# Optimization experiments

Hardware: AMD Instinct MI355X
Metric: run time of the kernel (lower is better)

## Reference

```python
import jax, jax.numpy as jnp
import numpy as np

EMBED_DIM = 1024
NUM_HEADS = 16
HEAD_DIM = EMBED_DIM // NUM_HEADS
SCALE = HEAD_DIM ** -0.5
B, S = 4, 2048


def setup_inputs() -> dict:
    key = jax.random.key(0)
    ks = jax.random.split(key, 11)
    std = EMBED_DIM ** -0.5
    return {
        "query": jax.random.normal(ks[0], (B, S, EMBED_DIM), jnp.float32),
        "key": jax.random.normal(ks[1], (B, S, EMBED_DIM), jnp.float32),
        "value": jax.random.normal(ks[2], (B, S, EMBED_DIM), jnp.float32),
        "Wq": jax.random.normal(ks[3], (EMBED_DIM, EMBED_DIM), jnp.float32) * std,
        "bq": jax.random.normal(ks[4], (EMBED_DIM,), jnp.float32) * 0.01,
        "Wk": jax.random.normal(ks[5], (EMBED_DIM, EMBED_DIM), jnp.float32) * std,
        "bk": jax.random.normal(ks[6], (EMBED_DIM,), jnp.float32) * 0.01,
        "Wv": jax.random.normal(ks[7], (EMBED_DIM, EMBED_DIM), jnp.float32) * std,
        "bv": jax.random.normal(ks[8], (EMBED_DIM,), jnp.float32) * 0.01,
        "Wo": jax.random.normal(ks[9], (EMBED_DIM, EMBED_DIM), jnp.float32) * std,
        "bo": jax.random.normal(ks[10], (EMBED_DIM,), jnp.float32) * 0.01,
    }


def reference(query, key, value, Wq, bq, Wk, bk, Wv, bv, Wo, bo):
    b, s, _ = query.shape
    # torch.nn.Linear: x @ W.T + b
    q = query @ Wq.T + bq
    k = key @ Wk.T + bk
    v = value @ Wv.T + bv
    # [b, h, s, d]
    q = q.reshape(b, s, NUM_HEADS, HEAD_DIM).transpose(0, 2, 1, 3)
    k = k.reshape(b, s, NUM_HEADS, HEAD_DIM).transpose(0, 2, 1, 3)
    v = v.reshape(b, s, NUM_HEADS, HEAD_DIM).transpose(0, 2, 1, 3)
    # explicit scores [b, h, s, s]
    scores = jnp.einsum("bhqd,bhkd->bhqk", q, k) * SCALE
    causal = jnp.tril(jnp.ones((s, s), dtype=bool))  # is_causal=True
    scores = jnp.where(causal, scores, -jnp.inf)
    attn = jax.nn.softmax(scores, axis=-1)
    out = jnp.einsum("bhqk,bhkd->bhqd", attn, v)
    out = out.transpose(0, 2, 1, 3).reshape(b, s, EMBED_DIM)
    return out @ Wo.T + bo
```

## Files before the change

kernel.cpp:

```cpp
#include <hip/hip_runtime.h>


#define E 1024
#define HEADS 16
#define HD 64
#define SEQ 2048
#define BATCH 4
#define MROWS (BATCH * SEQ)

typedef __bf16 bf16x8 __attribute__((ext_vector_type(8)));
typedef __bf16 bf16x2 __attribute__((ext_vector_type(2)));
typedef float f32x4 __attribute__((ext_vector_type(4)));
typedef unsigned short ushort8v __attribute__((ext_vector_type(8)));

typedef __attribute__((address_space(1))) void gvoid;
typedef __attribute__((address_space(3))) void lvoid;

__device__ __forceinline__ void async16(const void* g, void* l) {
  __builtin_amdgcn_global_load_lds((gvoid*)g, (lvoid*)l, 16, 0, 0);
}

__device__ __forceinline__ unsigned short f2bf(float f) {
  union { float f; unsigned int u; } v;
  v.f = f;
  unsigned int r = v.u + 0x7FFFu + ((v.u >> 16) & 1u);
  return (unsigned short)(r >> 16);
}

__device__ __forceinline__ unsigned packbf(float a, float b) {
  bf16x2 t;
  t[0] = (__bf16)a;
  t[1] = (__bf16)b;
  return __builtin_bit_cast(unsigned, t);
}

__device__ __forceinline__ void store_out(unsigned short* p, float v) { *p = f2bf(v); }
__device__ __forceinline__ void store_out(float* p, float v) { *p = v; }

struct CastArgs {
  const float* src[4];
  unsigned short* dst[4];
  int n;
};

__global__ __launch_bounds__(256) void cast_kernel(CastArgs a) {
  const float* s = a.src[blockIdx.z];
  unsigned short* d = a.dst[blockIdx.z];
  const int n = a.n;
  const int stride = gridDim.x * blockDim.x * 4;
  for (int i = (blockIdx.x * blockDim.x + threadIdx.x) * 4; i < n; i += stride) {
    float4 v = *(const float4*)(s + i);
    ushort4 o;
    o.x = f2bf(v.x); o.y = f2bf(v.y); o.z = f2bf(v.z); o.w = f2bf(v.w);
    *(ushort4*)(d + i) = o;
  }
}

template <typename OutT>
__device__ __forceinline__ void gemm_body(const unsigned short* __restrict__ A,
                                          const unsigned short* __restrict__ W,
                                          const float* __restrict__ bias,
                                          OutT* __restrict__ out, float scale) {
  __shared__ unsigned short At[128 * 64];
  __shared__ unsigned short Wt[128 * 64];
  const int tid = threadIdx.x;
  const int lane = tid & 63;
  const int wv = tid >> 6;
  const int wm = wv & 1, wn = wv >> 1;
  const int li = lane & 15, g = lane >> 4;
  const int m0 = blockIdx.x * 128, n0 = blockIdx.y * 128;
  f32x4 acc[4][4] = {};

  for (int k0 = 0; k0 < E; k0 += 64) {
    __syncthreads();
#pragma unroll
    for (int i = 0; i < 4; ++i) {
      int c = tid + 256 * i;
      int row = c >> 3, slot = c & 7;
      int gc = slot ^ (row & 7);
      async16(A + (size_t)(m0 + row) * E + k0 + gc * 8, &At[c * 8]);
      async16(W + (size_t)(n0 + row) * E + k0 + gc * 8, &Wt[c * 8]);
    }
    asm volatile("s_waitcnt vmcnt(0)" ::: "memory");
    __syncthreads();
#pragma unroll
    for (int kk = 0; kk < 2; ++kk) {
      bf16x8 af[4], bfr[4];
#pragma unroll
      for (int mt = 0; mt < 4; ++mt) {
        int r = wm * 64 + mt * 16 + li;
        int slot = (kk * 4 + g) ^ (r & 7);
        af[mt] = *(const bf16x8*)&At[r * 64 + slot * 8];
      }
#pragma unroll
      for (int nt = 0; nt < 4; ++nt) {
        int r = wn * 64 + nt * 16 + li;
        int slot = (kk * 4 + g) ^ (r & 7);
        bfr[nt] = *(const bf16x8*)&Wt[r * 64 + slot * 8];
      }
#pragma unroll
      for (int mt = 0; mt < 4; ++mt)
#pragma unroll
        for (int nt = 0; nt < 4; ++nt)
          acc[mt][nt] =
              __builtin_amdgcn_mfma_f32_16x16x32_bf16(af[mt], bfr[nt], acc[mt][nt], 0, 0, 0);
    }
  }

#pragma unroll
  for (int nt = 0; nt < 4; ++nt) {
    int col = n0 + wn * 64 + nt * 16 + li;
    float bv = bias[col];
#pragma unroll
    for (int mt = 0; mt < 4; ++mt) {
#pragma unroll
      for (int r = 0; r < 4; ++r) {
        int row = m0 + wm * 64 + mt * 16 + g * 4 + r;
        store_out(&out[(size_t)row * E + col], (acc[mt][nt][r] + bv) * scale);
      }
    }
  }
}

struct QkvArgs {
  const unsigned short* A[3];
  const unsigned short* W[3];
  const float* bias[3];
  unsigned short* out[3];
  float scale[3];
};

__global__ __launch_bounds__(256) void gemm_qkv(QkvArgs p) {
  const int z = blockIdx.z;
  gemm_body<unsigned short>(p.A[z], p.W[z], p.bias[z], p.out[z], p.scale[z]);
}

__global__ __launch_bounds__(256) void gemm_out_k(const unsigned short* __restrict__ A,
                                                  const unsigned short* __restrict__ W,
                                                  const float* __restrict__ bias,
                                                  float* __restrict__ out) {
  gemm_body<float>(A, W, bias, out, 1.0f);
}

__global__ __launch_bounds__(256, 2) void flash_kernel(const unsigned short* __restrict__ Qb,
                                                       const unsigned short* __restrict__ Kb,
                                                       const unsigned short* __restrict__ Vb,
                                                       unsigned short* __restrict__ Ob) {
  __shared__ unsigned short Kt[2][128 * 64];
  __shared__ unsigned short Vt[2][64 * 128];
  const int p = blockIdx.x;
  const int bh = blockIdx.y;
  const int b = bh >> 4, h16 = bh & 15;
  const size_t base = (size_t)b * SEQ * E + (size_t)h16 * HD;
  const unsigned short* Qp = Qb + base;
  const unsigned short* Kp = Kb + base;
  const unsigned short* Vp = Vb + base;
  unsigned short* Op = Ob + base;
  const int tid = threadIdx.x, lane = tid & 63, wv = tid >> 6;
  const int li = lane & 15, g = lane >> 4;
  const int qlo = p, qhi = 15 - p;
  const int slo = ((g & 1) << 5) | li;

  bf16x8 qfL[2][2], qfH[2][2];
#pragma unroll
  for (int mt = 0; mt < 2; ++mt)
#pragma unroll
    for (int kk = 0; kk < 2; ++kk) {
      int rl = qlo * 128 + wv * 32 + mt * 16 + li;
      int rh = qhi * 128 + wv * 32 + mt * 16 + li;
      qfL[mt][kk] = *(const bf16x8*)(Qp + (size_t)rl * E + kk * 32 + g * 8);
      qfH[mt][kk] = *(const bf16x8*)(Qp + (size_t)rh * E + kk * 32 + g * 8);
    }

  f32x4 oaL[4][2] = {}, oaH[4][2] = {};
  float miL[2] = {-1e30f, -1e30f}, lsL[2] = {0.0f, 0.0f};
  float miH[2] = {-1e30f, -1e30f}, lsH[2] = {0.0f, 0.0f};

  ushort8v vv[4];

  auto loadV = [&](int j) {
#pragma unroll
    for (int i = 0; i < 4; ++i) {
      int c = tid + 256 * i;
      int key = c & 127, db = (c >> 7) * 8;
      vv[i] = *(const ushort8v*)(Vp + (size_t)(j * 128 + key) * E + db);
    }
  };
  auto stageK = [&](int j, int buf) {
#pragma unroll
    for (int i = 0; i < 4; ++i) {
      int c = tid + 256 * i;
      int row = c >> 3, slot = c & 7;
      int gc = slot ^ (row & 7);
      async16(Kp + (size_t)(j * 128 + row) * E + gc * 8, &Kt[buf][c * 8]);
    }
  };
  auto scatV = [&](int buf) {
#pragma unroll
    for (int i = 0; i < 4; ++i) {
      int c = tid + 256 * i;
      int key = c & 127, db = (c >> 7) * 8;
#pragma unroll
      for (int jj = 0; jj < 8; ++jj) {
        int n = db + jj;
        int slot = (key >> 3) ^ (n & 15);
        Vt[buf][n * 128 + slot * 8 + (key & 7)] = vv[i][jj];
      }
    }
  };

  auto compute = [&](const bf16x8 (&qf)[2][2], float (&mi)[2], float (&ls)[2],
                     f32x4 (&oa)[4][2], bool diag, int buf) {
#pragma unroll
    for (int h = 0; h < 2; ++h) {
      if (diag && h * 64 > wv * 32 + 31) continue;

      f32x4 sacc[4][2] = {};
#pragma unroll
      for (int kk = 0; kk < 2; ++kk) {
        bf16x8 kf[4];
#pragma unroll
        for (int nt = 0; nt < 4; ++nt) {
          int key = h * 64 + nt * 16 + li;
          int slot = (kk * 4 + g) ^ (key & 7);
          kf[nt] = *(const bf16x8*)&Kt[buf][key * 64 + slot * 8];
        }
#pragma unroll
        for (int nt = 0; nt < 4; ++nt)
#pragma unroll
          for (int mt = 0; mt < 2; ++mt)
            sacc[nt][mt] =
                __builtin_amdgcn_mfma_f32_16x16x32_bf16(kf[nt], qf[mt][kk], sacc[nt][mt], 0, 0, 0);
      }

      if (diag && h * 64 + 63 > wv * 32) {
#pragma unroll
        for (int nt = 0; nt < 4; ++nt)
#pragma unroll
          for (int mt = 0; mt < 2; ++mt)
#pragma unroll
            for (int r = 0; r < 4; ++r) {
              int keyg = h * 64 + nt * 16 + g * 4 + r;
              int qg = wv * 32 + mt * 16 + li;
              sacc[nt][mt][r] = (keyg > qg) ? -1e30f : sacc[nt][mt][r];
            }
      }

      float alpha[2];
#pragma unroll
      for (int mt = 0; mt < 2; ++mt) {
        float mx = sacc[0][mt][0];
#pragma unroll
        for (int nt = 0; nt < 4; ++nt)
#pragma unroll
          for (int r = 0; r < 4; ++r) mx = fmaxf(mx, sacc[nt][mt][r]);
        mx = fmaxf(mx, __shfl_xor(mx, 16));
        mx = fmaxf(mx, __shfl_xor(mx, 32));
        float mnew = fmaxf(mi[mt], mx);
        alpha[mt] = __expf(mi[mt] - mnew);
        mi[mt] = mnew;
      }

      unsigned pk[4][2][2];
      float rs[2] = {0.0f, 0.0f};
#pragma unroll
      for (int nt = 0; nt < 4; ++nt)
#pragma unroll
        for (int mt = 0; mt < 2; ++mt) {
          float p0 = __expf(sacc[nt][mt][0] - mi[mt]);
          float p1 = __expf(sacc[nt][mt][1] - mi[mt]);
          float p2 = __expf(sacc[nt][mt][2] - mi[mt]);
          float p3 = __expf(sacc[nt][mt][3] - mi[mt]);
          rs[mt] += (p0 + p1) + (p2 + p3);
          pk[nt][mt][0] = packbf(p0, p1);
          pk[nt][mt][1] = packbf(p2, p3);
        }
#pragma unroll
      for (int mt = 0; mt < 2; ++mt) {
        float s = rs[mt];
        s += __shfl_xor(s, 16);
        s += __shfl_xor(s, 32);
        ls[mt] = ls[mt] * alpha[mt] + s;
#pragma unroll
        for (int dt = 0; dt < 4; ++dt) oa[dt][mt] *= alpha[mt];
      }

#pragma unroll
      for (int kk2 = 0; kk2 < 2; ++kk2) {
        const int kc = h * 2 + kk2;
        bf16x8 vf[4];
#pragma unroll
        for (int dt = 0; dt < 4; ++dt) {
          int d = dt * 16 + li;
          int slot = (kc * 4 + g) ^ (d & 15);
          vf[dt] = *(const bf16x8*)&Vt[buf][d * 128 + slot * 8];
        }
#pragma unroll
        for (int mt = 0; mt < 2; ++mt) {
          int a0 = __shfl((int)pk[kk2 * 2][mt][0], slo);
          int a1 = __shfl((int)pk[kk2 * 2][mt][1], slo);
          int a2 = __shfl((int)pk[kk2 * 2][mt][0], slo + 16);
          int a3 = __shfl((int)pk[kk2 * 2][mt][1], slo + 16);
          int c0 = __shfl((int)pk[kk2 * 2 + 1][mt][0], slo);
          int c1 = __shfl((int)pk[kk2 * 2 + 1][mt][1], slo);
          int c2 = __shfl((int)pk[kk2 * 2 + 1][mt][0], slo + 16);
          int c3 = __shfl((int)pk[kk2 * 2 + 1][mt][1], slo + 16);
          bool hi = (g & 2) != 0;
          uint4 bb;
          bb.x = hi ? c0 : a0;
          bb.y = hi ? c1 : a1;
          bb.z = hi ? c2 : a2;
          bb.w = hi ? c3 : a3;
          bf16x8 pf = __builtin_bit_cast(bf16x8, bb);
#pragma unroll
          for (int dt = 0; dt < 4; ++dt)
            oa[dt][mt] =
                __builtin_amdgcn_mfma_f32_16x16x32_bf16(vf[dt], pf, oa[dt][mt], 0, 0, 0);
        }
      }
    }
  };

  loadV(0);
  stageK(0, 0);
  scatV(0);

  for (int j = 0; j <= qhi; ++j) {
    const int buf = j & 1;
    asm volatile("s_waitcnt vmcnt(0)" ::: "memory");
    __syncthreads();
    if (j < qhi) {
      loadV(j + 1);
      stageK(j + 1, buf ^ 1);
    }
    compute(qfH, miH, lsH, oaH, j == qhi, buf);
    if (j <= qlo) compute(qfL, miL, lsL, oaL, j == qlo, buf);
    if (j < qhi) scatV(buf ^ 1);
  }

#pragma unroll
  for (int t = 0; t < 2; ++t) {
    const int qt = t ? qhi : qlo;
    f32x4(&oa)[4][2] = t ? oaH : oaL;
    float* ls = t ? lsH : lsL;
#pragma unroll
    for (int mt = 0; mt < 2; ++mt) {
      float inv = 1.0f / ls[mt];
      int row = qt * 128 + wv * 32 + mt * 16 + li;
#pragma unroll
      for (int dt = 0; dt < 4; ++dt) {
        ushort4 w;
        w.x = f2bf(oa[dt][mt][0] * inv);
        w.y = f2bf(oa[dt][mt][1] * inv);
        w.z = f2bf(oa[dt][mt][2] * inv);
        w.w = f2bf(oa[dt][mt][3] * inv);
        *(ushort4*)(Op + (size_t)row * E + dt * 16 + g * 4) = w;
      }
    }
  }
}

extern "C" void kernel_launch(void* const* d_in, const int* in_sizes, int n_in,
                              void* d_out, int out_size, void* d_ws, size_t ws_size,
                              hipStream_t stream) {
  const float* q  = (const float*)d_in[0];
  const float* k  = (const float*)d_in[1];
  const float* v  = (const float*)d_in[2];
  const float* Wq = (const float*)d_in[3];
  const float* bq = (const float*)d_in[4];
  const float* Wk = (const float*)d_in[5];
  const float* bk = (const float*)d_in[6];
  const float* Wv = (const float*)d_in[7];
  const float* bv = (const float*)d_in[8];
  const float* Wo = (const float*)d_in[9];
  const float* bo = (const float*)d_in[10];

  unsigned short* Xq  = (unsigned short*)d_ws;
  unsigned short* Xk  = Xq + (size_t)MROWS * E;
  unsigned short* Xv  = Xk + (size_t)MROWS * E;
  unsigned short* Wqb = Xv + (size_t)MROWS * E;
  unsigned short* Wkb = Wqb + (size_t)E * E;
  unsigned short* Wvb = Wkb + (size_t)E * E;
  unsigned short* Wob = Wvb + (size_t)E * E;
  unsigned short* Qb  = Wob + (size_t)E * E;
  unsigned short* Kb  = Qb + (size_t)MROWS * E;
  unsigned short* Vb  = Kb + (size_t)MROWS * E;
  unsigned short* Og  = Xq;

  CastArgs ca;
  ca.src[0] = q; ca.src[1] = k; ca.src[2] = v; ca.src[3] = nullptr;
  ca.dst[0] = Xq; ca.dst[1] = Xk; ca.dst[2] = Xv; ca.dst[3] = nullptr;
  ca.n = MROWS * E;
  cast_kernel<<<dim3(1024, 1, 3), 256, 0, stream>>>(ca);

  CastArgs cw;
  cw.src[0] = Wq; cw.src[1] = Wk; cw.src[2] = Wv; cw.src[3] = Wo;
  cw.dst[0] = Wqb; cw.dst[1] = Wkb; cw.dst[2] = Wvb; cw.dst[3] = Wob;
  cw.n = E * E;
  cast_kernel<<<dim3(256, 1, 4), 256, 0, stream>>>(cw);

  QkvArgs p;
  p.A[0] = Xq;  p.A[1] = Xk;  p.A[2] = Xv;
  p.W[0] = Wqb; p.W[1] = Wkb; p.W[2] = Wvb;
  p.bias[0] = bq; p.bias[1] = bk; p.bias[2] = bv;
  p.out[0] = Qb; p.out[1] = Kb; p.out[2] = Vb;
  p.scale[0] = 0.125f; p.scale[1] = 1.0f; p.scale[2] = 1.0f;
  gemm_qkv<<<dim3(64, 8, 3), 256, 0, stream>>>(p);

  flash_kernel<<<dim3(8, 64), 256, 0, stream>>>(Qb, Kb, Vb, Og);

  gemm_out_k<<<dim3(64, 8), 256, 0, stream>>>(Og, Wob, bo, (float*)d_out);
}
```

Measured before the change: 404.3 us.

## Split flash attention query tile across 8 waves of 16 rows each

The flash kernel block grows from 256 to 512 threads, so each wave handles 16 query rows instead of 32 (one M-tile instead of two), with K/V staging loops halved per thread. This cuts per-wave register use (accumulators, Q fragments, softmax state) and raises the occupancy target to 4 blocks per CU. In exchange, each K/V LDS fragment read is reused across fewer MFMAs, adding LDS traffic per FLOP, and more waves share each barrier.

```diff
diff --git a/kernel.cpp b/kernel.cpp
--- a/kernel.cpp
+++ b/kernel.cpp
@@ -142,7 +142,7 @@
   gemm_body<float>(A, W, bias, out, 1.0f);
 }
 
-__global__ __launch_bounds__(256, 2) void flash_kernel(const unsigned short* __restrict__ Qb,
+__global__ __launch_bounds__(512, 4) void flash_kernel(const unsigned short* __restrict__ Qb,
                                                        const unsigned short* __restrict__ Kb,
                                                        const unsigned short* __restrict__ Vb,
                                                        unsigned short* __restrict__ Ob) {
@@ -161,35 +161,33 @@
   const int qlo = p, qhi = 15 - p;
   const int slo = ((g & 1) << 5) | li;
 
-  bf16x8 qfL[2][2], qfH[2][2];
-#pragma unroll
-  for (int mt = 0; mt < 2; ++mt)
-#pragma unroll
-    for (int kk = 0; kk < 2; ++kk) {
-      int rl = qlo * 128 + wv * 32 + mt * 16 + li;
-      int rh = qhi * 128 + wv * 32 + mt * 16 + li;
-      qfL[mt][kk] = *(const bf16x8*)(Qp + (size_t)rl * E + kk * 32 + g * 8);
-      qfH[mt][kk] = *(const bf16x8*)(Qp + (size_t)rh * E + kk * 32 + g * 8);
-    }
-
-  f32x4 oaL[4][2] = {}, oaH[4][2] = {};
-  float miL[2] = {-1e30f, -1e30f}, lsL[2] = {0.0f, 0.0f};
-  float miH[2] = {-1e30f, -1e30f}, lsH[2] = {0.0f, 0.0f};
-
-  ushort8v vv[4];
+  bf16x8 qfL[2], qfH[2];
+#pragma unroll
+  for (int kk = 0; kk < 2; ++kk) {
+    int rl = qlo * 128 + wv * 16 + li;
+    int rh = qhi * 128 + wv * 16 + li;
+    qfL[kk] = *(const bf16x8*)(Qp + (size_t)rl * E + kk * 32 + g * 8);
+    qfH[kk] = *(const bf16x8*)(Qp + (size_t)rh * E + kk * 32 + g * 8);
+  }
+
+  f32x4 oaL[4] = {}, oaH[4] = {};
+  float miL = -1e30f, lsL = 0.0f;
+  float miH = -1e30f, lsH = 0.0f;
+
+  ushort8v vv[2];
 
   auto loadV = [&](int j) {
 #pragma unroll
-    for (int i = 0; i < 4; ++i) {
-      int c = tid + 256 * i;
+    for (int i = 0; i < 2; ++i) {
+      int c = tid + 512 * i;
       int key = c & 127, db = (c >> 7) * 8;
       vv[i] = *(const ushort8v*)(Vp + (size_t)(j * 128 + key) * E + db);
     }
   };
   auto stageK = [&](int j, int buf) {
 #pragma unroll
-    for (int i = 0; i < 4; ++i) {
-      int c = tid + 256 * i;
+    for (int i = 0; i < 2; ++i) {
+      int c = tid + 512 * i;
       int row = c >> 3, slot = c & 7;
       int gc = slot ^ (row & 7);
       async16(Kp + (size_t)(j * 128 + row) * E + gc * 8, &Kt[buf][c * 8]);
@@ -197,8 +195,8 @@
   };
   auto scatV = [&](int buf) {
 #pragma unroll
-    for (int i = 0; i < 4; ++i) {
-      int c = tid + 256 * i;
+    for (int i = 0; i < 2; ++i) {
+      int c = tid + 512 * i;
       int key = c & 127, db = (c >> 7) * 8;
 #pragma unroll
       for (int jj = 0; jj < 8; ++jj) {
@@ -209,13 +207,13 @@
     }
   };
 
-  auto compute = [&](const bf16x8 (&qf)[2][2], float (&mi)[2], float (&ls)[2],
-                     f32x4 (&oa)[4][2], bool diag, int buf) {
+  auto compute = [&](const bf16x8 (&qf)[2], float& mi, float& ls,
+                     f32x4 (&oa)[4], bool diag, int buf) {
 #pragma unroll
     for (int h = 0; h < 2; ++h) {
-      if (diag && h * 64 > wv * 32 + 31) continue;
-
-      f32x4 sacc[4][2] = {};
+      if (diag && h * 64 > wv * 16 + 15) continue;
+
+      f32x4 sacc[4] = {};
 #pragma unroll
       for (int kk = 0; kk < 2; ++kk) {
         bf16x8 kf[4];
@@ -227,62 +225,51 @@
         }
 #pragma unroll
         for (int nt = 0; nt < 4; ++nt)
-#pragma unroll
-          for (int mt = 0; mt < 2; ++mt)
-            sacc[nt][mt] =
-                __builtin_amdgcn_mfma_f32_16x16x32_bf16(kf[nt], qf[mt][kk], sacc[nt][mt], 0, 0, 0);
-      }
-
-      if (diag && h * 64 + 63 > wv * 32) {
+          sacc[nt] =
+              __builtin_amdgcn_mfma_f32_16x16x32_bf16(kf[nt], qf[kk], sacc[nt], 0, 0, 0);
+      }
+
+      if (diag && h * 64 + 63 > wv * 16) {
 #pragma unroll
         for (int nt = 0; nt < 4; ++nt)
 #pragma unroll
-          for (int mt = 0; mt < 2; ++mt)
-#pragma unroll
-            for (int r = 0; r < 4; ++r) {
-              int keyg = h * 64 + nt * 16 + g * 4 + r;
-              int qg = wv * 32 + mt * 16 + li;
-              sacc[nt][mt][r] = (keyg > qg) ? -1e30f : sacc[nt][mt][r];
-            }
-      }
-
-      float alpha[2];
-#pragma unroll
-      for (int mt = 0; mt < 2; ++mt) {
-        float mx = sacc[0][mt][0];
-#pragma unroll
-        for (int nt = 0; nt < 4; ++nt)
-#pragma unroll
-          for (int r = 0; r < 4; ++r) mx = fmaxf(mx, sacc[nt][mt][r]);
-        mx = fmaxf(mx, __shfl_xor(mx, 16));
-        mx = fmaxf(mx, __shfl_xor(mx, 32));
-        float mnew = fmaxf(mi[mt], mx);
-        alpha[mt] = __expf(mi[mt] - mnew);
-        mi[mt] = mnew;
-      }
-
-      unsigned pk[4][2][2];
-      float rs[2] = {0.0f, 0.0f};
+          for (int r = 0; r < 4; ++r) {
+            int keyg = h * 64 + nt * 16 + g * 4 + r;
+            int qg = wv * 16 + li;
+            sacc[nt][r] = (keyg > qg) ? -1e30f : sacc[nt][r];
+          }
+      }
+
+      float mx = sacc[0][0];
 #pragma unroll
       for (int nt = 0; nt < 4; ++nt)
 #pragma unroll
-        for (int mt = 0; mt < 2; ++mt) {
-          float p0 = __expf(sacc[nt][mt][0] - mi[mt]);
-          float p1 = __expf(sacc[nt][mt][1] - mi[mt]);
-          float p2 = __expf(sacc[nt][mt][2] - mi[mt]);
-          float p3 = __expf(sacc[nt][mt][3] - mi[mt]);
-          rs[mt] += (p0 + p1) + (p2 + p3);
-          pk[nt][mt][0] = packbf(p0, p1);
-          pk[nt][mt][1] = packbf(p2, p3);
-        }
-#pragma unroll
-      for (int mt = 0; mt < 2; ++mt) {
-        float s = rs[mt];
+        for (int r = 0; r < 4; ++r) mx = fmaxf(mx, sacc[nt][r]);
+      mx = fmaxf(mx, __shfl_xor(mx, 16));
+      mx = fmaxf(mx, __shfl_xor(mx, 32));
+      float mnew = fmaxf(mi, mx);
+      float alpha = __expf(mi - mnew);
+      mi = mnew;
+
+      unsigned pk[4][2];
+      float rs = 0.0f;
+#pragma unroll
+      for (int nt = 0; nt < 4; ++nt) {
+        float p0 = __expf(sacc[nt][0] - mi);
+        float p1 = __expf(sacc[nt][1] - mi);
+        float p2 = __expf(sacc[nt][2] - mi);
+        float p3 = __expf(sacc[nt][3] - mi);
+        rs += (p0 + p1) + (p2 + p3);
+        pk[nt][0] = packbf(p0, p1);
+        pk[nt][1] = packbf(p2, p3);
+      }
+      {
+        float s = rs;
         s += __shfl_xor(s, 16);
         s += __shfl_xor(s, 32);
-        ls[mt] = ls[mt] * alpha[mt] + s;
-#pragma unroll
-        for (int dt = 0; dt < 4; ++dt) oa[dt][mt] *= alpha[mt];
+        ls = ls * alpha + s;
+#pragma unroll
+        for (int dt = 0; dt < 4; ++dt) oa[dt] *= alpha;
       }
 
 #pragma unroll
@@ -295,28 +282,25 @@
           int slot = (kc * 4 + g) ^ (d & 15);
           vf[dt] = *(const bf16x8*)&Vt[buf][d * 128 + slot * 8];
         }
-#pragma unroll
-        for (int mt = 0; mt < 2; ++mt) {
-          int a0 = __shfl((int)pk[kk2 * 2][mt][0], slo);
-          int a1 = __shfl((int)pk[kk2 * 2][mt][1], slo);
-          int a2 = __shfl((int)pk[kk2 * 2][mt][0], slo + 16);
-          int a3 = __shfl((int)pk[kk2 * 2][mt][1], slo + 16);
-          int c0 = __shfl((int)pk[kk2 * 2 + 1][mt][0], slo);
-          int c1 = __shfl((int)pk[kk2 * 2 + 1][mt][1], slo);
-          int c2 = __shfl((int)pk[kk2 * 2 + 1][mt][0], slo + 16);
-          int c3 = __shfl((int)pk[kk2 * 2 + 1][mt][1], slo + 16);
-          bool hi = (g & 2) != 0;
-          uint4 bb;
-          bb.x = hi ? c0 : a0;
-          bb.y = hi ? c1 : a1;
-          bb.z = hi ? c2 : a2;
-          bb.w = hi ? c3 : a3;
-          bf16x8 pf = __builtin_bit_cast(bf16x8, bb);
-#pragma unroll
-          for (int dt = 0; dt < 4; ++dt)
-            oa[dt][mt] =
-                __builtin_amdgcn_mfma_f32_16x16x32_bf16(vf[dt], pf, oa[dt][mt], 0, 0, 0);
-        }
+        int a0 = __shfl((int)pk[kk2 * 2][0], slo);
+        int a1 = __shfl((int)pk[kk2 * 2][1], slo);
+        int a2 = __shfl((int)pk[kk2 * 2][0], slo + 16);
+        int a3 = __shfl((int)pk[kk2 * 2][1], slo + 16);
+        int c0 = __shfl((int)pk[kk2 * 2 + 1][0], slo);
+        int c1 = __shfl((int)pk[kk2 * 2 + 1][1], slo);
+        int c2 = __shfl((int)pk[kk2 * 2 + 1][0], slo + 16);
+        int c3 = __shfl((int)pk[kk2 * 2 + 1][1], slo + 16);
+        bool hi = (g & 2) != 0;
+        uint4 bb;
+        bb.x = hi ? c0 : a0;
+        bb.y = hi ? c1 : a1;
+        bb.z = hi ? c2 : a2;
+        bb.w = hi ? c3 : a3;
+        bf16x8 pf = __builtin_bit_cast(bf16x8, bb);
+#pragma unroll
+        for (int dt = 0; dt < 4; ++dt)
+          oa[dt] =
+              __builtin_amdgcn_mfma_f32_16x16x32_bf16(vf[dt], pf, oa[dt], 0, 0, 0);
       }
     }
   };
@@ -341,21 +325,18 @@
 #pragma unroll
   for (int t = 0; t < 2; ++t) {
     const int qt = t ? qhi : qlo;
-    f32x4(&oa)[4][2] = t ? oaH : oaL;
-    float* ls = t ? lsH : lsL;
-#pragma unroll
-    for (int mt = 0; mt < 2; ++mt) {
-      float inv = 1.0f / ls[mt];
-      int row = qt * 128 + wv * 32 + mt * 16 + li;
-#pragma unroll
-      for (int dt = 0; dt < 4; ++dt) {
-        ushort4 w;
-        w.x = f2bf(oa[dt][mt][0] * inv);
-        w.y = f2bf(oa[dt][mt][1] * inv);
-        w.z = f2bf(oa[dt][mt][2] * inv);
-        w.w = f2bf(oa[dt][mt][3] * inv);
-        *(ushort4*)(Op + (size_t)row * E + dt * 16 + g * 4) = w;
-      }
+    f32x4(&oa)[4] = t ? oaH : oaL;
+    float ls = t ? lsH : lsL;
+    float inv = 1.0f / ls;
+    int row = qt * 128 + wv * 16 + li;
+#pragma unroll
+    for (int dt = 0; dt < 4; ++dt) {
+      ushort4 w;
+      w.x = f2bf(oa[dt][0] * inv);
+      w.y = f2bf(oa[dt][1] * inv);
+      w.z = f2bf(oa[dt][2] * inv);
+      w.w = f2bf(oa[dt][3] * inv);
+      *(ushort4*)(Op + (size_t)row * E + dt * 16 + g * 4) = w;
     }
   }
 }
@@ -407,7 +388,7 @@
   p.scale[0] = 0.125f; p.scale[1] = 1.0f; p.scale[2] = 1.0f;
   gemm_qkv<<<dim3(64, 8, 3), 256, 0, stream>>>(p);
 
-  flash_kernel<<<dim3(8, 64), 256, 0, stream>>>(Qb, Kb, Vb, Og);
+  flash_kernel<<<dim3(8, 64), 512, 0, stream>>>(Qb, Kb, Vb, Og);
 
   gemm_out_k<<<dim3(64, 8), 256, 0, stream>>>(Og, Wob, bo, (float*)d_out);
 }
```

Result: no change. 402.0 us (-0.6%).
